# Optimization experiments

Hardware: AMD Instinct MI355X
Metric: run time of the kernel (lower is better)

The kernel has to match this reference:

```python
import jax, jax.numpy as jnp
from jax import lax
import numpy as np

# Quantization params from the torch module
IN_SCALE, IN_ZP = 0.01, 7
W_SCALE, W_ZP = 0.01, 3
B_SCALE = 0.0001
INT32_MIN, INT32_MAX = -2147483648.0, 2147483647.0


def setup_inputs() -> dict:
    key = jax.random.key(0)
    k1, k2, k3 = jax.random.split(key, 3)
    # int8-valued tensors stored as int32 (int8 range [-128, 127])
    inputVec = jax.random.randint(k1, (64, 16, 256, 256), -128, 128, dtype=jnp.int32)
    weight = jax.random.randint(k2, (16, 16, 3, 3), -128, 128, dtype=jnp.int32)
    bias = jax.random.normal(k3, (16,), dtype=jnp.float32)
    return {"inputVec": inputVec, "weight": weight, "bias": bias, "groups": 1}


def reference(inputVec, weight, bias, groups):
    # per-tensor dequantize: (q - zero_point) * scale
    x = (inputVec.astype(jnp.float32) - IN_ZP) * IN_SCALE          # [N, Cin, H, W]
    w = (weight.astype(jnp.float32) - W_ZP) * W_SCALE              # [Cout, Cin/g, kH, kW]
    # bias: quantize to qint32 (zp=0) then dequantize (round-half-to-even, clamp to int32)
    b = jnp.clip(jnp.round(bias / B_SCALE), INT32_MIN, INT32_MAX) * B_SCALE
    out = lax.conv_general_dilated(
        x, w,
        window_strides=(1, 1),
        padding='VALID',
        dimension_numbers=('NCHW', 'OIHW', 'NCHW'),
        feature_group_count=groups,
    )
    return out + b[None, :, None, None]
```

## Files before the change

### kernel.cpp

```cpp
#include <hip/hip_runtime.h>

#define H 256
#define W 256
#define CIN 16
#define COUT 16
#define OH 254
#define OW 254
#define OHB 12
#define IRB (OHB + 2)
#define COLS 259
#define NOHG 22

typedef int int4v __attribute__((ext_vector_type(4)));

__global__ __launch_bounds__(256, 2) void conv_q8_mfma(
    const int* __restrict__ x, const int* __restrict__ wq,
    const float* __restrict__ bias, float* __restrict__ out)
{
    __shared__ int4v lds_x[IRB * COLS];
    __shared__ int4v lds_wA[192];
    __shared__ int   lds_ci[COUT];
    __shared__ float lds_bf[COUT];

    const int tid = threadIdx.x;
    const int ohg = blockIdx.x;
    const int n   = blockIdx.y;
    const int oh0 = ohg * OHB;

    for (int t = tid; t < 192; t += 256) {
        const int co = t & 15;
        const int kw = (t >> 4) & 3;
        const int kh = t >> 6;
        int4v pk = {0, 0, 0, 0};
        if (kw < 3) {
#pragma unroll
            for (int q = 0; q < 4; ++q) {
                int r = 0;
#pragma unroll
                for (int b = 0; b < 4; ++b) {
                    const int cin = q * 4 + b;
                    r |= (wq[((co * CIN + cin) * 3 + kh) * 3 + kw] & 0xff) << (8 * b);
                }
                pk[q] = r;
            }
        }
        lds_wA[t] = pk;
    }
    if (tid < COUT) {
        int s = 0;
        const int* wc = wq + tid * CIN * 9;
#pragma unroll
        for (int k = 0; k < CIN * 9; ++k) s += wc[k];
        lds_ci[tid] = -7 * s + 144 * 21;
        float r = rintf(bias[tid] * 10000.0f);
        r = fminf(fmaxf(r, -2147483648.0f), 2147483647.0f);
        lds_bf[tid] = r * 1e-4f;
    }

    const int* xn = x + (size_t)n * (CIN * H * W);
    for (int t = tid; t < IRB * COLS; t += 256) {
        const int row = t / COLS;
        const int col = t - row * COLS;
        int4v pk = {0, 0, 0, 0};
        if (col < W) {
            int ih = oh0 + row;
            if (ih > H - 1) ih = H - 1;
            const int* p = xn + ih * W + col;
#pragma unroll
            for (int q = 0; q < 4; ++q) {
                int r = 0;
#pragma unroll
                for (int b = 0; b < 4; ++b)
                    r |= (p[(q * 4 + b) * (H * W)] & 0xff) << (8 * b);
                pk[q] = r;
            }
        }
        lds_x[t] = pk;
    }
    __syncthreads();

    const int wave = tid >> 6;
    const int lane = tid & 63;
    const int n16  = lane & 15;
    const int quad = lane >> 4;

    const int4v a0 = lds_wA[(0 * 4 + quad) * 16 + n16];
    const int4v a1 = lds_wA[(1 * 4 + quad) * 16 + n16];
    const int4v a2 = lds_wA[(2 * 4 + quad) * 16 + n16];
    const int ov = (quad < 3) ? 0x01010101 : 0;
    const int4v aones = {ov, ov, ov, ov};

    int   ci_r[4];
    float bf_r[4];
#pragma unroll
    for (int r = 0; r < 4; ++r) {
        ci_r[r] = lds_ci[quad * 4 + r];
        bf_r[r] = lds_bf[quad * 4 + r];
    }

    float* outn = out + (size_t)n * (COUT * OH * OW);
    const int coff = n16 + quad;

#pragma unroll
    for (int i = 0; i < 3; ++i) {
        const int rl = wave * 3 + i;
        const int oh = oh0 + rl;
        if (oh >= OH) continue;
        for (int g = 0; g < 16; ++g) {
            const int ow0 = g * 16;
            const int c = ow0 + coff;
            const int4v b0 = lds_x[(rl + 0) * COLS + c];
            const int4v b1 = lds_x[(rl + 1) * COLS + c];
            const int4v b2 = lds_x[(rl + 2) * COLS + c];
            int4v acc = {0, 0, 0, 0};
            int4v acs = {0, 0, 0, 0};
            acc = __builtin_amdgcn_mfma_i32_16x16x64_i8(a0, b0, acc, 0, 0, 0);
            acc = __builtin_amdgcn_mfma_i32_16x16x64_i8(a1, b1, acc, 0, 0, 0);
            acc = __builtin_amdgcn_mfma_i32_16x16x64_i8(a2, b2, acc, 0, 0, 0);
            acs = __builtin_amdgcn_mfma_i32_16x16x64_i8(aones, b0, acs, 0, 0, 0);
            acs = __builtin_amdgcn_mfma_i32_16x16x64_i8(aones, b1, acs, 0, 0, 0);
            acs = __builtin_amdgcn_mfma_i32_16x16x64_i8(aones, b2, acs, 0, 0, 0);
            const int sx = acs[0];
            const int ow = ow0 + n16;
            if (ow < OW) {
#pragma unroll
                for (int r = 0; r < 4; ++r) {
                    const int co  = quad * 4 + r;
                    const int tot = acc[r] - 3 * sx + ci_r[r];
                    outn[(co * OH + oh) * OW + ow] = fmaf(1e-4f, (float)tot, bf_r[r]);
                }
            }
        }
    }
}

extern "C" void kernel_launch(void* const* d_in, const int* in_sizes, int n_in,
                              void* d_out, int out_size, void* d_ws, size_t ws_size,
                              hipStream_t stream) {
    const int*   x    = (const int*)d_in[0];
    const int*   wq   = (const int*)d_in[1];
    const float* bias = (const float*)d_in[2];
    float*       out  = (float*)d_out;

    const int n = in_sizes[0] / (CIN * H * W);
    dim3 grid(NOHG, n);
    conv_q8_mfma<<<grid, 256, 0, stream>>>(x, wq, bias, out);
}
```

Measured before the change: 481.2 us.

## Double block threads, vectorize input staging loads, and pack bytes with perm

```diff
diff --git a/kernel.cpp b/kernel.cpp
--- a/kernel.cpp
+++ b/kernel.cpp
@@ -10,10 +10,21 @@
 #define IRB (OHB + 2)
 #define COLS 259
 #define NOHG 22
+#define NTHREADS 512
+#define NWAVES 8
+#define TILES (OHB * 16)
+#define TPW (TILES / NWAVES)
 
 typedef int int4v __attribute__((ext_vector_type(4)));
+typedef int int2v __attribute__((ext_vector_type(2)));
 
-__global__ __launch_bounds__(256, 2) void conv_q8_mfma(
+static __device__ __forceinline__ int pack4(int d0, int d1, int d2, int d3) {
+    int t0 = __builtin_amdgcn_perm(d1, d0, 0x00000400);
+    int t1 = __builtin_amdgcn_perm(d3, d2, 0x00000400);
+    return __builtin_amdgcn_perm(t1, t0, 0x05040100);
+}
+
+__global__ __launch_bounds__(NTHREADS, 4) void conv_q8_mfma(
     const int* __restrict__ x, const int* __restrict__ wq,
     const float* __restrict__ bias, float* __restrict__ out)
 {
@@ -27,7 +38,8 @@
     const int n   = blockIdx.y;
     const int oh0 = ohg * OHB;
 
-    for (int t = tid; t < 192; t += 256) {
+    if (tid < 192) {
+        const int t = tid;
         const int co = t & 15;
         const int kw = (t >> 4) & 3;
         const int kh = t >> 6;
@@ -35,13 +47,8 @@
         if (kw < 3) {
 #pragma unroll
             for (int q = 0; q < 4; ++q) {
-                int r = 0;
-#pragma unroll
-                for (int b = 0; b < 4; ++b) {
-                    const int cin = q * 4 + b;
-                    r |= (wq[((co * CIN + cin) * 3 + kh) * 3 + kw] & 0xff) << (8 * b);
-                }
-                pk[q] = r;
+                const int* wp = wq + ((co * CIN + q * 4) * 3 + kh) * 3 + kw;
+                pk[q] = pack4(wp[0], wp[9], wp[18], wp[27]);
             }
         }
         lds_wA[t] = pk;
@@ -56,26 +63,31 @@
         r = fminf(fmaxf(r, -2147483648.0f), 2147483647.0f);
         lds_bf[tid] = r * 1e-4f;
     }
+    if (tid < IRB * 4) {
+        const int row = tid >> 2;
+        const int col = 256 + (tid & 3);
+        if (col < COLS) lds_x[row * COLS + col] = (int4v){0, 0, 0, 0};
+    }
 
     const int* xn = x + (size_t)n * (CIN * H * W);
-    for (int t = tid; t < IRB * COLS; t += 256) {
-        const int row = t / COLS;
-        const int col = t - row * COLS;
-        int4v pk = {0, 0, 0, 0};
-        if (col < W) {
-            int ih = oh0 + row;
-            if (ih > H - 1) ih = H - 1;
-            const int* p = xn + ih * W + col;
+    for (int t = tid; t < IRB * 128; t += NTHREADS) {
+        const int row = t >> 7;
+        const int c2 = (t & 127) * 2;
+        int ih = oh0 + row;
+        if (ih > H - 1) ih = H - 1;
+        const int* p = xn + ih * W + c2;
+        int4v pk0, pk1;
 #pragma unroll
-            for (int q = 0; q < 4; ++q) {
-                int r = 0;
-#pragma unroll
-                for (int b = 0; b < 4; ++b)
-                    r |= (p[(q * 4 + b) * (H * W)] & 0xff) << (8 * b);
-                pk[q] = r;
-            }
+        for (int q = 0; q < 4; ++q) {
+            const int2v d0 = *(const int2v*)(p + (q * 4 + 0) * (H * W));
+            const int2v d1 = *(const int2v*)(p + (q * 4 + 1) * (H * W));
+            const int2v d2 = *(const int2v*)(p + (q * 4 + 2) * (H * W));
+            const int2v d3 = *(const int2v*)(p + (q * 4 + 3) * (H * W));
+            pk0[q] = pack4(d0.x, d1.x, d2.x, d3.x);
+            pk1[q] = pack4(d0.y, d1.y, d2.y, d3.y);
         }
-        lds_x[t] = pk;
+        lds_x[row * COLS + c2]     = pk0;
+        lds_x[row * COLS + c2 + 1] = pk1;
     }
     __syncthreads();
 
@@ -101,34 +113,32 @@
     float* outn = out + (size_t)n * (COUT * OH * OW);
     const int coff = n16 + quad;
 
-#pragma unroll
-    for (int i = 0; i < 3; ++i) {
-        const int rl = wave * 3 + i;
+    for (int t = wave * TPW; t < wave * TPW + TPW; ++t) {
+        const int rl = t >> 4;
+        const int g  = t & 15;
         const int oh = oh0 + rl;
         if (oh >= OH) continue;
-        for (int g = 0; g < 16; ++g) {
-            const int ow0 = g * 16;
-            const int c = ow0 + coff;
-            const int4v b0 = lds_x[(rl + 0) * COLS + c];
-            const int4v b1 = lds_x[(rl + 1) * COLS + c];
-            const int4v b2 = lds_x[(rl + 2) * COLS + c];
-            int4v acc = {0, 0, 0, 0};
-            int4v acs = {0, 0, 0, 0};
-            acc = __builtin_amdgcn_mfma_i32_16x16x64_i8(a0, b0, acc, 0, 0, 0);
-            acc = __builtin_amdgcn_mfma_i32_16x16x64_i8(a1, b1, acc, 0, 0, 0);
-            acc = __builtin_amdgcn_mfma_i32_16x16x64_i8(a2, b2, acc, 0, 0, 0);
-            acs = __builtin_amdgcn_mfma_i32_16x16x64_i8(aones, b0, acs, 0, 0, 0);
-            acs = __builtin_amdgcn_mfma_i32_16x16x64_i8(aones, b1, acs, 0, 0, 0);
-            acs = __builtin_amdgcn_mfma_i32_16x16x64_i8(aones, b2, acs, 0, 0, 0);
-            const int sx = acs[0];
-            const int ow = ow0 + n16;
-            if (ow < OW) {
+        const int ow0 = g * 16;
+        const int c = ow0 + coff;
+        const int4v b0 = lds_x[(rl + 0) * COLS + c];
+        const int4v b1 = lds_x[(rl + 1) * COLS + c];
+        const int4v b2 = lds_x[(rl + 2) * COLS + c];
+        int4v acc = {0, 0, 0, 0};
+        int4v acs = {0, 0, 0, 0};
+        acc = __builtin_amdgcn_mfma_i32_16x16x64_i8(a0, b0, acc, 0, 0, 0);
+        acc = __builtin_amdgcn_mfma_i32_16x16x64_i8(a1, b1, acc, 0, 0, 0);
+        acc = __builtin_amdgcn_mfma_i32_16x16x64_i8(a2, b2, acc, 0, 0, 0);
+        acs = __builtin_amdgcn_mfma_i32_16x16x64_i8(aones, b0, acs, 0, 0, 0);
+        acs = __builtin_amdgcn_mfma_i32_16x16x64_i8(aones, b1, acs, 0, 0, 0);
+        acs = __builtin_amdgcn_mfma_i32_16x16x64_i8(aones, b2, acs, 0, 0, 0);
+        const int sx = acs[0];
+        const int ow = ow0 + n16;
+        if (ow < OW) {
 #pragma unroll
-                for (int r = 0; r < 4; ++r) {
-                    const int co  = quad * 4 + r;
-                    const int tot = acc[r] - 3 * sx + ci_r[r];
-                    outn[(co * OH + oh) * OW + ow] = fmaf(1e-4f, (float)tot, bf_r[r]);
-                }
+            for (int r = 0; r < 4; ++r) {
+                const int co  = quad * 4 + r;
+                const int tot = acc[r] - 3 * sx + ci_r[r];
+                outn[(co * OH + oh) * OW + ow] = fmaf(1e-4f, (float)tot, bf_r[r]);
             }
         }
     }
@@ -144,5 +154,5 @@
 
     const int n = in_sizes[0] / (CIN * H * W);
     dim3 grid(NOHG, n);
-    conv_q8_mfma<<<grid, 256, 0, stream>>>(x, wq, bias, out);
+    conv_q8_mfma<<<grid, NTHREADS, 0, stream>>>(x, wq, bias, out);
 }
```

After: 476.7 us. No clear change (-1.0%).
